# Kernel optimization log

Measured on AMD Instinct MI355X. Metric: run time of the kernel, lower is better.

Reference implementation:

```python
import math
import jax, jax.numpy as jnp
import numpy as np

N_KERNELS = 2000
KERNEL_SIZES = (7, 9, 11)
SIG_LEN = 32768
K_MAX = 11
N_SAMPLES = 2


def gen_meta():
    """Mirrors RocketNet.__generate_random_kernels with a fixed seed.
    Returns per-kernel (k, dilation, padding), padded weights [N_KERNELS, K_MAX], biases [N_KERNELS]."""
    rng = np.random.RandomState(0)
    meta = []
    W = np.zeros((N_KERNELS, K_MAX), np.float32)
    b = np.zeros((N_KERNELS,), np.float32)
    for i in range(N_KERNELS):
        k = int(rng.choice(KERNEL_SIZES))
        max_dil = math.log2((SIG_LEN - 1) / (k - 1))
        e = int(rng.randint(0, int(max_dil)))
        d = int(2 ** e)
        p = 0 if rng.rand() <= 0.5 else int((k - 1) * d / 2)
        b[i] = rng.uniform(-1.0, 1.0)
        w = rng.normal(0.0, 1.0, size=k).astype(np.float32)
        W[i, :k] = w - w.mean()
        meta.append((k, d, p))
    return meta, W, b


def group_meta(meta):
    """Group kernel indices by identical (k, dilation, padding) so each group
    runs as a single multi-output-channel dilated conv (same math as the loop)."""
    groups = {}
    for i, (k, d, p) in enumerate(meta):
        groups.setdefault((k, d, p), []).append(i)
    return sorted(groups.items())


def setup_inputs() -> dict:
    key = jax.random.key(0)
    signal = jax.random.normal(key, (N_SAMPLES, SIG_LEN), dtype=jnp.float32)
    _, W, b = gen_meta()
    return {"signal": signal, "weights": jnp.asarray(W), "biases": jnp.asarray(b)}


def reference(signal, weights, biases):
    meta, _, _ = gen_meta()  # static per-kernel (k, d, p); weights come from args
    groups = group_meta(meta)
    x = signal[:, None, :]  # [n, 1, L]
    outs = []
    for (k, d, p), idx in groups:
        idx = np.asarray(idx)
        w = weights[idx, :k][:, None, :]  # [g, 1, k] (OIH)
        y = jax.lax.conv_general_dilated(
            x, w,
            window_strides=(1,),
            padding=[(p, p)],
            rhs_dilation=(d,),
            dimension_numbers=("NCH", "OIH", "NCH"),
        )  # [n, g, L_out]
        outs.append(y + biases[idx][None, :, None])
    return tuple(outs)
```

## Files before the change

kernel.cpp:

```cpp
#include <hip/hip_runtime.h>
#include <cstdint>
#include <cmath>
#include <cstring>
#include <map>
#include <tuple>
#include <vector>

#define SIG_LEN 32768
#define N_KERNELS 2000
#define NJOBS (N_KERNELS * 2)
#define TILES 32
#define TILE_W 1024

struct JobP { int out_base; unsigned packed; };

namespace nprng {
struct MT {
  uint32_t key[624]; int pos; bool has_gauss;
  void seed(uint32_t s) {
    for (int i = 0; i < 624; i++) { key[i] = s; s = 1812433253u * (s ^ (s >> 30)) + (uint32_t)i + 1u; }
    pos = 624; has_gauss = false;
  }
  void gen() {
    const uint32_t UM = 0x80000000u, LM = 0x7fffffffu, MA = 0x9908b0dfu;
    for (int i = 0; i < 624; i++) {
      uint32_t y = (key[i] & UM) | (key[(i + 1) % 624] & LM);
      key[i] = key[(i + 397) % 624] ^ (y >> 1) ^ ((y & 1u) ? MA : 0u);
    }
    pos = 0;
  }
  uint32_t next32() {
    if (pos == 624) gen();
    uint32_t y = key[pos++];
    y ^= y >> 11; y ^= (y << 7) & 0x9d2c5680u; y ^= (y << 15) & 0xefc60000u; y ^= y >> 18;
    return y;
  }
  double nextD() {
    uint32_t a = next32() >> 5, b = next32() >> 6;
    return ((double)a * 67108864.0 + (double)b) / 9007199254740992.0;
  }
  uint32_t bounded(uint32_t rng) {
    uint32_t mask = rng;
    mask |= mask >> 1; mask |= mask >> 2; mask |= mask >> 4;
    mask |= mask >> 8; mask |= mask >> 16;
    uint32_t v;
    do { v = next32() & mask; } while (v > rng);
    return v;
  }
  void consume_gauss(int n) {
    for (int i = 0; i < n; i++) {
      if (has_gauss) { has_gauss = false; continue; }
      double x1, x2, r2;
      do {
        x1 = 2.0 * nextD() - 1.0;
        x2 = 2.0 * nextD() - 1.0;
        r2 = x1 * x1 + x2 * x2;
      } while (r2 >= 1.0 || r2 == 0.0);
      has_gauss = true;
    }
  }
};
}

static JobP g_jobs[NJOBS];

static void build_jobs() {
  nprng::MT mt; mt.seed(0);
  static const int KS[3] = {7, 9, 11};
  int K[N_KERNELS], D[N_KERNELS], P[N_KERNELS], E[N_KERNELS];
  for (int i = 0; i < N_KERNELS; i++) {
    int k = KS[(int)mt.bounded(2)];
    int M = (int)std::log2((double)(SIG_LEN - 1) / (double)(k - 1));
    int e = (int)mt.bounded((uint32_t)(M - 1));
    int d = 1 << e;
    double r = mt.nextD();
    int p = (r <= 0.5) ? 0 : ((k - 1) * d / 2);
    mt.nextD();
    mt.consume_gauss(k);
    K[i] = k; D[i] = d; P[i] = p; E[i] = e;
  }
  std::map<std::tuple<int, int, int>, std::vector<int>> groups;
  for (int i = 0; i < N_KERNELS; i++)
    groups[std::make_tuple(K[i], D[i], P[i])].push_back(i);
  long long off = 0; int jn = 0;
  for (auto& kv : groups) {
    int k = std::get<0>(kv.first), d = std::get<1>(kv.first), p = std::get<2>(kv.first);
    int out_len = SIG_LEN + 2 * p - d * (k - 1);
    int ng = (int)kv.second.size();
    for (int c = 0; c < ng; c++) {
      int i = kv.second[c];
      int kcode = (k - 7) / 2;
      for (int n = 0; n < 2; n++) {
        g_jobs[jn].out_base = (int)(off + (long long)(n * ng + c) * out_len);
        g_jobs[jn].packed = (unsigned)i | ((unsigned)kcode << 11) | ((unsigned)E[i] << 13)
                          | ((unsigned)(p ? 1 : 0) << 17) | ((unsigned)n << 18);
        jn++;
      }
    }
    off += 2LL * ng * out_len;
  }
}

template <int K>
__device__ __forceinline__ void conv_run(const float* __restrict__ xs,
                                         const float* __restrict__ wrow, float bias,
                                         int d, int p, int out_len, int tbase,
                                         float* __restrict__ op) {
  float w[K];
#pragma unroll
  for (int q = 0; q < K; q++) w[q] = wrow[q];
  int tid = threadIdx.x;
  bool fast = (tbase + TILE_W <= out_len) && (tbase >= p) &&
              (tbase + (TILE_W - 1) + (K - 1) * d - p < SIG_LEN);
  if (fast) {
    const float* xp = xs + (tbase + tid - p);
    float a0 = bias, a1 = bias, a2 = bias, a3 = bias;
#pragma unroll
    for (int q = 0; q < K; q++) {
      a0 += w[q] * xp[0];
      a1 += w[q] * xp[256];
      a2 += w[q] * xp[512];
      a3 += w[q] * xp[768];
      xp += d;
    }
    float* o = op + tbase + tid;
    __builtin_nontemporal_store(a0, o);
    __builtin_nontemporal_store(a1, o + 256);
    __builtin_nontemporal_store(a2, o + 512);
    __builtin_nontemporal_store(a3, o + 768);
  } else {
#pragma unroll
    for (int s = 0; s < 4; s++) {
      int t = tbase + tid + s * 256;
      if (t < out_len) {
        float acc = bias;
#pragma unroll
        for (int q = 0; q < K; q++) {
          int idx = t + q * d - p;
          if ((unsigned)idx < (unsigned)SIG_LEN) acc += w[q] * xs[idx];
        }
        __builtin_nontemporal_store(acc, op + t);
      }
    }
  }
}

__global__ __launch_bounds__(256) void rocket_kernel(const float* __restrict__ x,
                                                     const float* __restrict__ W,
                                                     const float* __restrict__ B,
                                                     const JobP* __restrict__ jobs,
                                                     float* __restrict__ out) {
  int jb = blockIdx.x >> 5;
  int tile = blockIdx.x & (TILES - 1);
  int out_base = __builtin_amdgcn_readfirstlane(jobs[jb].out_base);
  unsigned packed = (unsigned)__builtin_amdgcn_readfirstlane((int)jobs[jb].packed);
  int widx = packed & 2047;
  int kcode = (packed >> 11) & 3;
  int e = (packed >> 13) & 15;
  int pflag = (packed >> 17) & 1;
  int n = (packed >> 18) & 1;
  int k = 7 + 2 * kcode;
  int d = 1 << e;
  int p = pflag ? (((k - 1) * d) >> 1) : 0;
  int out_len = SIG_LEN + 2 * p - (k - 1) * d;
  int tbase = tile * TILE_W;
  if (tbase >= out_len) return;
  const float* xs = x + n * SIG_LEN;
  const float* wrow = W + widx * 11;
  float bias = B[widx];
  float* op = out + out_base;
  if (kcode == 0)      conv_run<7>(xs, wrow, bias, d, p, out_len, tbase, op);
  else if (kcode == 1) conv_run<9>(xs, wrow, bias, d, p, out_len, tbase, op);
  else                 conv_run<11>(xs, wrow, bias, d, p, out_len, tbase, op);
}

extern "C" void kernel_launch(void* const* d_in, const int* in_sizes, int n_in,
                              void* d_out, int out_size, void* d_ws, size_t ws_size,
                              hipStream_t stream) {
  build_jobs();
  const float* x = (const float*)d_in[0];
  const float* W = (const float*)d_in[1];
  const float* B = (const float*)d_in[2];
  JobP* jdev = (JobP*)d_ws;
  hipMemcpyAsync(jdev, g_jobs, sizeof(g_jobs), hipMemcpyHostToDevice, stream);
  rocket_kernel<<<dim3(NJOBS * TILES), dim3(256), 0, stream>>>(x, W, B, jdev, (float*)d_out);
}
```

Measured before the change: 687.1 us.

## Batch four same-config kernels per block and vectorize per-thread outputs

Jobs now group up to four kernels that share (k, dilation, padding), so each block loads each input value once and applies it to four weight sets, producing four output channels. Each thread now computes four consecutive outputs with float4 loads and float4 nontemporal stores instead of four strided scalars. The aim is fewer blocks, less redundant input traffic and wider memory transactions, in exchange for more registers per thread and possible misaligned vector accesses when dilation or padding is odd.

```diff
diff --git a/kernel.cpp b/kernel.cpp
--- a/kernel.cpp
+++ b/kernel.cpp
@@ -8,11 +8,12 @@
 
 #define SIG_LEN 32768
 #define N_KERNELS 2000
-#define NJOBS (N_KERNELS * 2)
 #define TILES 32
 #define TILE_W 1024
-
-struct JobP { int out_base; unsigned packed; };
+#define CCH 4
+#define MAXJOBS 2048
+
+struct JobC { int out_base; unsigned short widx[4]; unsigned meta; };
 
 namespace nprng {
 struct MT {
@@ -62,7 +63,8 @@
 };
 }
 
-static JobP g_jobs[NJOBS];
+static JobC g_jobs[MAXJOBS];
+static int g_njobs = 0;
 
 static void build_jobs() {
   nprng::MT mt; mt.seed(0);
@@ -86,60 +88,86 @@
   for (auto& kv : groups) {
     int k = std::get<0>(kv.first), d = std::get<1>(kv.first), p = std::get<2>(kv.first);
     int out_len = SIG_LEN + 2 * p - d * (k - 1);
-    int ng = (int)kv.second.size();
-    for (int c = 0; c < ng; c++) {
-      int i = kv.second[c];
-      int kcode = (k - 7) / 2;
-      for (int n = 0; n < 2; n++) {
-        g_jobs[jn].out_base = (int)(off + (long long)(n * ng + c) * out_len);
-        g_jobs[jn].packed = (unsigned)i | ((unsigned)kcode << 11) | ((unsigned)E[i] << 13)
-                          | ((unsigned)(p ? 1 : 0) << 17) | ((unsigned)n << 18);
-        jn++;
+    auto& v = kv.second;
+    int ng = (int)v.size();
+    int kcode = (k - 7) / 2;
+    int e = E[v[0]];
+    for (int n = 0; n < 2; n++) {
+      for (int c0 = 0; c0 < ng; c0 += CCH) {
+        int cact = (ng - c0 < CCH) ? (ng - c0) : CCH;
+        JobC& j = g_jobs[jn++];
+        j.out_base = (int)(off + (long long)(n * ng + c0) * out_len);
+        for (int c = 0; c < CCH; c++)
+          j.widx[c] = (unsigned short)v[c0 + (c < cact ? c : cact - 1)];
+        j.meta = (unsigned)kcode | ((unsigned)e << 2) | ((unsigned)(p ? 1 : 0) << 6)
+               | ((unsigned)n << 7) | ((unsigned)(cact - 1) << 8);
       }
     }
     off += 2LL * ng * out_len;
   }
-}
+  g_njobs = jn;
+}
+
+typedef float f4 __attribute__((ext_vector_type(4), aligned(4)));
 
 template <int K>
-__device__ __forceinline__ void conv_run(const float* __restrict__ xs,
-                                         const float* __restrict__ wrow, float bias,
-                                         int d, int p, int out_len, int tbase,
-                                         float* __restrict__ op) {
-  float w[K];
-#pragma unroll
-  for (int q = 0; q < K; q++) w[q] = wrow[q];
+__device__ __forceinline__ void conv4(const float* __restrict__ xs,
+                                      const float* __restrict__ W,
+                                      const float* __restrict__ B,
+                                      const int* widx, int cact,
+                                      int d, int p, int out_len, int tbase,
+                                      float* __restrict__ op) {
+  float w[CCH][K]; float bias[CCH];
+#pragma unroll
+  for (int c = 0; c < CCH; c++) {
+    const float* wr = W + widx[c] * 11;
+#pragma unroll
+    for (int q = 0; q < K; q++) w[c][q] = wr[q];
+    bias[c] = B[widx[c]];
+  }
   int tid = threadIdx.x;
+  int t0 = tbase + 4 * tid;
   bool fast = (tbase + TILE_W <= out_len) && (tbase >= p) &&
               (tbase + (TILE_W - 1) + (K - 1) * d - p < SIG_LEN);
   if (fast) {
-    const float* xp = xs + (tbase + tid - p);
-    float a0 = bias, a1 = bias, a2 = bias, a3 = bias;
+    const float* xp = xs + (t0 - p);
+    f4 a[CCH];
+#pragma unroll
+    for (int c = 0; c < CCH; c++) { a[c] = (f4){bias[c], bias[c], bias[c], bias[c]}; }
 #pragma unroll
     for (int q = 0; q < K; q++) {
-      a0 += w[q] * xp[0];
-      a1 += w[q] * xp[256];
-      a2 += w[q] * xp[512];
-      a3 += w[q] * xp[768];
+      f4 xv = *(const f4*)xp;
       xp += d;
-    }
-    float* o = op + tbase + tid;
-    __builtin_nontemporal_store(a0, o);
-    __builtin_nontemporal_store(a1, o + 256);
-    __builtin_nontemporal_store(a2, o + 512);
-    __builtin_nontemporal_store(a3, o + 768);
+#pragma unroll
+      for (int c = 0; c < CCH; c++) a[c] += w[c][q] * xv;
+    }
+#pragma unroll
+    for (int c = 0; c < CCH; c++) {
+      if (c < cact) {
+        float* o = op + c * out_len + t0;
+        __builtin_nontemporal_store(a[c], (f4*)o);
+      }
+    }
   } else {
 #pragma unroll
     for (int s = 0; s < 4; s++) {
-      int t = tbase + tid + s * 256;
+      int t = t0 + s;
       if (t < out_len) {
-        float acc = bias;
+        float acc[CCH];
+#pragma unroll
+        for (int c = 0; c < CCH; c++) acc[c] = bias[c];
 #pragma unroll
         for (int q = 0; q < K; q++) {
           int idx = t + q * d - p;
-          if ((unsigned)idx < (unsigned)SIG_LEN) acc += w[q] * xs[idx];
+          if ((unsigned)idx < (unsigned)SIG_LEN) {
+            float xv = xs[idx];
+#pragma unroll
+            for (int c = 0; c < CCH; c++) acc[c] += w[c][q] * xv;
+          }
         }
-        __builtin_nontemporal_store(acc, op + t);
+#pragma unroll
+        for (int c = 0; c < CCH; c++)
+          if (c < cact) __builtin_nontemporal_store(acc[c], op + c * out_len + t);
       }
     }
   }
@@ -148,17 +176,23 @@
 __global__ __launch_bounds__(256) void rocket_kernel(const float* __restrict__ x,
                                                      const float* __restrict__ W,
                                                      const float* __restrict__ B,
-                                                     const JobP* __restrict__ jobs,
+                                                     const JobC* __restrict__ jobs,
                                                      float* __restrict__ out) {
   int jb = blockIdx.x >> 5;
   int tile = blockIdx.x & (TILES - 1);
-  int out_base = __builtin_amdgcn_readfirstlane(jobs[jb].out_base);
-  unsigned packed = (unsigned)__builtin_amdgcn_readfirstlane((int)jobs[jb].packed);
-  int widx = packed & 2047;
-  int kcode = (packed >> 11) & 3;
-  int e = (packed >> 13) & 15;
-  int pflag = (packed >> 17) & 1;
-  int n = (packed >> 18) & 1;
+  const int4* jp = (const int4*)jobs;
+  int4 jraw = jp[jb];
+  int out_base = __builtin_amdgcn_readfirstlane(jraw.x);
+  int wp0 = __builtin_amdgcn_readfirstlane(jraw.y);
+  int wp1 = __builtin_amdgcn_readfirstlane(jraw.z);
+  unsigned meta = (unsigned)__builtin_amdgcn_readfirstlane(jraw.w);
+  int widx[CCH] = { wp0 & 0xffff, (wp0 >> 16) & 0xffff,
+                    wp1 & 0xffff, (wp1 >> 16) & 0xffff };
+  int kcode = meta & 3;
+  int e     = (meta >> 2) & 15;
+  int pflag = (meta >> 6) & 1;
+  int n     = (meta >> 7) & 1;
+  int cact  = ((meta >> 8) & 3) + 1;
   int k = 7 + 2 * kcode;
   int d = 1 << e;
   int p = pflag ? (((k - 1) * d) >> 1) : 0;
@@ -166,12 +200,10 @@
   int tbase = tile * TILE_W;
   if (tbase >= out_len) return;
   const float* xs = x + n * SIG_LEN;
-  const float* wrow = W + widx * 11;
-  float bias = B[widx];
   float* op = out + out_base;
-  if (kcode == 0)      conv_run<7>(xs, wrow, bias, d, p, out_len, tbase, op);
-  else if (kcode == 1) conv_run<9>(xs, wrow, bias, d, p, out_len, tbase, op);
-  else                 conv_run<11>(xs, wrow, bias, d, p, out_len, tbase, op);
+  if (kcode == 0)      conv4<7>(xs, W, B, widx, cact, d, p, out_len, tbase, op);
+  else if (kcode == 1) conv4<9>(xs, W, B, widx, cact, d, p, out_len, tbase, op);
+  else                 conv4<11>(xs, W, B, widx, cact, d, p, out_len, tbase, op);
 }
 
 extern "C" void kernel_launch(void* const* d_in, const int* in_sizes, int n_in,
@@ -181,7 +213,7 @@
   const float* x = (const float*)d_in[0];
   const float* W = (const float*)d_in[1];
   const float* B = (const float*)d_in[2];
-  JobP* jdev = (JobP*)d_ws;
+  JobC* jdev = (JobC*)d_ws;
   hipMemcpyAsync(jdev, g_jobs, sizeof(g_jobs), hipMemcpyHostToDevice, stream);
-  rocket_kernel<<<dim3(NJOBS * TILES), dim3(256), 0, stream>>>(x, W, B, jdev, (float*)d_out);
-}
+  rocket_kernel<<<dim3(g_njobs * TILES), dim3(256), 0, stream>>>(x, W, B, jdev, (float*)d_out);
+}
```

New measurement: 671.9 us. 1.02x faster.
